# Kernel optimization log

Hardware: AMD Instinct MI355X
Metric: run time of the kernel (lower is better)

The kernel has to match this reference:

```python
import jax, jax.numpy as jnp
import numpy as np
import math

SCALE = 64.0
MARGIN = 0.5
EPS = 1e-07
COS_M = math.cos(MARGIN)
SIN_M = math.sin(MARGIN)
THRESHOLD = math.cos(math.pi - MARGIN)
MM = math.sin(math.pi - MARGIN) * MARGIN

N, D, C = 512, 512, 100000


def setup_inputs() -> dict:
    key = jax.random.key(0)
    k1, k2, k3 = jax.random.split(key, 3)
    x = jax.random.normal(k1, (N, D), dtype=jnp.float32)
    weight = jax.random.normal(k2, (C, D), dtype=jnp.float32)
    t = jnp.zeros((1,), dtype=jnp.float32)
    target = jax.random.randint(k3, (N,), 0, C, dtype=jnp.int64)
    return {"x": x, "weight": weight, "t": t, "target": target}


def reference(x, weight, t, target):
    # normalized linear -> cosine similarities [N, C]
    xn = x / jnp.linalg.norm(x, axis=1, keepdims=True)
    wn = weight / jnp.linalg.norm(weight, axis=1, keepdims=True)
    cos_theta = jnp.clip(jnp.einsum('nd,cd->nc', xn, wn), -1.0 + EPS, 1.0 - EPS)

    rows = jnp.arange(cos_theta.shape[0])
    target_logit = cos_theta[rows, target][:, None]            # [N, 1]
    sin_theta = jnp.sqrt(1.0 - target_logit * target_logit)
    cos_theta_m = target_logit * COS_M - sin_theta * SIN_M      # cos(theta + m)

    mask = cos_theta > cos_theta_m                              # hard examples
    final_target_logit = jnp.where(target_logit > THRESHOLD,
                                   cos_theta_m,
                                   target_logit - MM)

    # EMA buffer update (no-grad in torch)
    t_new = jax.lax.stop_gradient(target_logit.mean() * 0.01 + 0.99 * t)  # [1]

    # hard-example re-weighting: cos * (t + cos) where mask
    cos_theta = jnp.where(mask, cos_theta * (t_new[0] + cos_theta), cos_theta)
    # scatter margin-adjusted target logit into target column
    cos_theta = cos_theta.at[rows, target].set(final_target_logit[:, 0])

    logits = cos_theta * SCALE
    # cross entropy (mean)
    logp = jax.nn.log_softmax(logits, axis=-1)
    loss = -jnp.mean(logp[rows, target])
    return loss
```

## Files before the change

kernel.cpp:

```cpp
#include <hip/hip_runtime.h>
#include <hip/hip_bf16.h>
#include <stdint.h>

#define N_ROWS 512
#define D_DIM  512
#define C_CLS  100000

#define SCALE_F    64.0f
#define EPS_F      1e-7f
#define COS_M_F    0.8775825618903728f
#define SIN_M_F    0.4794255386042030f
#define THRESH_F  -0.8775825618903728f
#define MM_F       0.2397127693021015f
#define FIXMAX_F   65.0f

#define NG 391

#define XN8_OFF    0
#define TL_OFF     (XN8_OFF + 512*512)
#define CTM_OFF    (TL_OFF + 2048)
#define FTL_OFF    (CTM_OFF + 2048)
#define TNEW_OFF   (FTL_OFF + 2048)
#define XNORM_OFF  (TNEW_OFF + 256)
#define PSUM_OFF   (XNORM_OFF + 2048)
#define LOSSI_OFF  (PSUM_OFF + 512*NG*4)
#define WNB8_OFF   (LOSSI_OFF + 2048)

typedef __attribute__((ext_vector_type(4))) float f32x4;

#define GLOAD_LDS16(gp, lp) \
    __builtin_amdgcn_global_load_lds((const __attribute__((address_space(1))) void*)(gp), \
                                     (__attribute__((address_space(3))) void*)(lp), 16, 0, 0)

#if defined(__has_builtin)
#if __has_builtin(__builtin_amdgcn_cvt_pk_fp8_f32)
#define HAVE_CVT_FP8 1
#endif
#endif

__device__ inline unsigned char f2e4m3(float f) {
    union { float f; unsigned u; } a; a.f = f;
    unsigned s = (a.u >> 24) & 0x80u;
    float af = fabsf(f);
    if (af < 0.015625f) {
        int q = (int)(af * 512.0f + 0.5f);
        return (unsigned char)(s | (unsigned)q);
    }
    unsigned x = a.u & 0x7FFFFFFFu;
    unsigned r = x + 0x000FFFFFu + ((x >> 20) & 1u);
    int ec = (int)(r >> 23) - 127 + 7;
    unsigned m = (r >> 20) & 7u;
    if (ec > 15 || (ec == 15 && m == 7u)) return (unsigned char)(s | 0x7Eu);
    return (unsigned char)(s | ((unsigned)ec << 3) | m);
}

__device__ inline uint2 pack8_fp8(float f0, float f1, float f2, float f3,
                                  float f4, float f5, float f6, float f7) {
#ifdef HAVE_CVT_FP8
    int w0 = __builtin_amdgcn_cvt_pk_fp8_f32(f0, f1, 0, false);
    w0     = __builtin_amdgcn_cvt_pk_fp8_f32(f2, f3, w0, true);
    int w1 = __builtin_amdgcn_cvt_pk_fp8_f32(f4, f5, 0, false);
    w1     = __builtin_amdgcn_cvt_pk_fp8_f32(f6, f7, w1, true);
    uint2 r; r.x = (unsigned)w0; r.y = (unsigned)w1;
    return r;
#else
    union { unsigned char b[8]; uint2 q; } u;
    u.b[0]=f2e4m3(f0); u.b[1]=f2e4m3(f1); u.b[2]=f2e4m3(f2); u.b[3]=f2e4m3(f3);
    u.b[4]=f2e4m3(f4); u.b[5]=f2e4m3(f5); u.b[6]=f2e4m3(f6); u.b[7]=f2e4m3(f7);
    return u.q;
#endif
}

__device__ inline float wave_sum64(float v) {
    #pragma unroll
    for (int m = 1; m < 64; m <<= 1) v += __shfl_xor(v, m);
    return v;
}

__global__ void k_xnorm_fp8(const float* __restrict__ x,
                            unsigned char* __restrict__ xn8,
                            float* __restrict__ xnorm) {
    int row = blockIdx.x;
    int lane = threadIdx.x;
    const float* xr = x + row * D_DIM + lane * 8;
    float4 v0 = *(const float4*)(xr);
    float4 v1 = *(const float4*)(xr + 4);
    float s = v0.x*v0.x + v0.y*v0.y + v0.z*v0.z + v0.w*v0.w
            + v1.x*v1.x + v1.y*v1.y + v1.z*v1.z + v1.w*v1.w;
    s = wave_sum64(s);
    float nrm = sqrtf(s);
    if (lane == 0) xnorm[row] = nrm;
    float inv = 1.0f / nrm;
    uint2 q = pack8_fp8(v0.x*inv, v0.y*inv, v0.z*inv, v0.w*inv,
                        v1.x*inv, v1.y*inv, v1.z*inv, v1.w*inv);
    *(uint2*)(xn8 + row * D_DIM + lane * 8) = q;
}

__global__ void k_wnorm_fp8(const float* __restrict__ w,
                            unsigned char* __restrict__ wnb8) {
    int row = blockIdx.x * 4 + (threadIdx.x >> 6);
    int lane = threadIdx.x & 63;
    if (row < C_CLS) {
        const float* wr = w + (size_t)row * D_DIM + lane * 8;
        f32x4 v0 = __builtin_nontemporal_load((const f32x4*)(wr));
        f32x4 v1 = __builtin_nontemporal_load((const f32x4*)(wr + 4));
        float s = v0.x*v0.x + v0.y*v0.y + v0.z*v0.z + v0.w*v0.w
                + v1.x*v1.x + v1.y*v1.y + v1.z*v1.z + v1.w*v1.w;
        s = wave_sum64(s);
        float inv = rsqrtf(s);
        uint2 q = pack8_fp8(v0.x*inv, v0.y*inv, v0.z*inv, v0.w*inv,
                            v1.x*inv, v1.y*inv, v1.z*inv, v1.w*inv);
        *(uint2*)(wnb8 + (size_t)row * D_DIM + lane * 8) = q;
    } else {
        uint2 z = {0u, 0u};
        *(uint2*)(wnb8 + (size_t)row * D_DIM + lane * 8) = z;
    }
}

__global__ void k_tlogit(const float* __restrict__ x, const float* __restrict__ w,
                         const float* __restrict__ xnorm,
                         const int* __restrict__ target,
                         float* __restrict__ tl, float* __restrict__ ctm,
                         float* __restrict__ ftl) {
    int row = blockIdx.x;
    int lane = threadIdx.x;
    int tgt = target[row];
    const float* xr = x + row * D_DIM + lane * 8;
    const float* wr = w + (size_t)tgt * D_DIM + lane * 8;
    float4 a0 = *(const float4*)(xr),     a1 = *(const float4*)(xr + 4);
    float4 b0 = *(const float4*)(wr),     b1 = *(const float4*)(wr + 4);
    float s = a0.x*b0.x + a0.y*b0.y + a0.z*b0.z + a0.w*b0.w
            + a1.x*b1.x + a1.y*b1.y + a1.z*b1.z + a1.w*b1.w;
    float q = b0.x*b0.x + b0.y*b0.y + b0.z*b0.z + b0.w*b0.w
            + b1.x*b1.x + b1.y*b1.y + b1.z*b1.z + b1.w*b1.w;
    s = wave_sum64(s);
    q = wave_sum64(q);
    if (lane == 0) {
        float c = s / (xnorm[row] * sqrtf(q));
        c = fminf(fmaxf(c, -1.0f + EPS_F), 1.0f - EPS_F);
        float sn = sqrtf(fmaxf(1.0f - c * c, 0.0f));
        float cm = c * COS_M_F - sn * SIN_M_F;
        tl[row]  = c;
        ctm[row] = cm;
        ftl[row] = (c > THRESH_F) ? cm : (c - MM_F);
    }
}

__global__ void k_tnew(const float* __restrict__ tl, const float* __restrict__ t,
                       float* __restrict__ tnew) {
    __shared__ float s[512];
    int tid = threadIdx.x;
    s[tid] = tl[tid];
    __syncthreads();
    for (int off = 256; off > 0; off >>= 1) {
        if (tid < off) s[tid] += s[tid + off];
        __syncthreads();
    }
    if (tid == 0) tnew[0] = (s[0] / 512.0f) * 0.01f + 0.99f * t[0];
}

__global__ __launch_bounds__(512) void k_gemm_fp8(
        const unsigned char* __restrict__ xn8,
        const unsigned char* __restrict__ wnb8,
        const int* __restrict__ target,
        const float* __restrict__ ctm,
        const float* __restrict__ ftl,
        const float* __restrict__ tnew,
        float* __restrict__ psum) {
    __shared__ unsigned char As[64 * 512];
    __shared__ int   tgt_s[64];
    __shared__ float ctm_s[64];
    __shared__ float ftl_s[64];
    __shared__ float redS[8][64];

    int bx = blockIdx.x;
    int logical = (bx & 7) * 391 + (bx >> 3);
    int ng = logical >> 3, mb = logical & 7;
    int rowbase = mb * 64;

    int tid = threadIdx.x;
    int lane = tid & 63, wid = tid >> 6;
    int fr = lane & 15, rgrp = lane >> 4;
    int cb = ng * 256 + wid * 32;

    if (tid < 64) {
        int rg = rowbase + tid;
        tgt_s[tid] = target[rg];
        ctm_s[tid] = ctm[rg];
        ftl_s[tid] = ftl[rg];
    }

    const unsigned char* bptr[2];
    bool cvalid[2];
    #pragma unroll
    for (int j = 0; j < 2; j++) {
        int cgl = cb + j * 16 + fr;
        cvalid[j] = (cgl < C_CLS);
        bptr[j] = wnb8 + (size_t)cgl * D_DIM + rgrp * 8;
    }

    uint2 bv[6][2];
    #pragma unroll
    for (int d = 0; d < 6; d++)
        #pragma unroll
        for (int j = 0; j < 2; j++)
            bv[d][j] = *(const uint2*)(bptr[j] + d * 32);

    #pragma unroll
    for (int c2 = 0; c2 < 4; ++c2) {
        int lo = wid * 4096 + c2 * 1024;
        int o  = lo + lane * 16;
        int row = o >> 9;
        int b   = (o & 511) ^ ((row & 7) << 4);
        GLOAD_LDS16(xn8 + (size_t)(rowbase + row) * 512 + b, (char*)As + lo);
    }
    __syncthreads();

    float tn = tnew[0];
    int key = (fr & 7) << 4;

    f32x4 acc[4][2];
    #pragma unroll
    for (int m = 0; m < 4; m++)
        #pragma unroll
        for (int j = 0; j < 2; j++)
            acc[m][j] = (f32x4){0.f, 0.f, 0.f, 0.f};

    union LL { uint2 u; long long ll; };

    uint2 af[2][4];
    #pragma unroll
    for (int m = 0; m < 4; m++)
        af[0][m] = *(const uint2*)(As + (m * 16 + fr) * 512 + ((rgrp * 8) ^ key));

    #pragma unroll
    for (int kk = 0; kk < 16; ++kk) {
        int cur = kk & 1;
        if (kk < 15) {
            #pragma unroll
            for (int m = 0; m < 4; m++)
                af[cur ^ 1][m] = *(const uint2*)(As + (m * 16 + fr) * 512
                                 + (((kk + 1) * 32 + rgrp * 8) ^ key));
        }
        if (kk < 10) {
            #pragma unroll
            for (int j = 0; j < 2; j++)
                bv[(kk + 6) % 6][j] = *(const uint2*)(bptr[j] + (kk + 6) * 32);
        }
        __builtin_amdgcn_s_setprio(1);
        #pragma unroll
        for (int m = 0; m < 4; m++)
            #pragma unroll
            for (int j = 0; j < 2; j++) {
                LL a, b;
                a.u = af[cur][m];
                b.u = bv[kk % 6][j];
                acc[m][j] = __builtin_amdgcn_mfma_f32_16x16x32_fp8_fp8(
                                a.ll, b.ll, acc[m][j], 0, 0, 0);
            }
        __builtin_amdgcn_s_setprio(0);
    }

    #pragma unroll
    for (int m = 0; m < 4; m++) {
        #pragma unroll
        for (int reg = 0; reg < 4; reg++) {
            int rl = m * 16 + rgrp * 4 + reg;
            int tr = tgt_s[rl];
            float cm = ctm_s[rl];
            float ft = ftl_s[rl];
            float sm = 0.0f;
            #pragma unroll
            for (int j = 0; j < 2; j++) {
                int col = cb + j * 16 + fr;
                float c = acc[m][j][reg];
                c = fminf(fmaxf(c, -1.0f + EPS_F), 1.0f - EPS_F);
                float v = (c > cm) ? c * (tn + c) : c;
                v *= SCALE_F;
                v = (col == tr) ? ft * SCALE_F : v;
                v = cvalid[j] ? v : -3.0e38f;
                sm += __expf(v - FIXMAX_F);
            }
            #pragma unroll
            for (int msk = 1; msk < 16; msk <<= 1) sm += __shfl_xor(sm, msk);
            if (fr == 0) redS[wid][rl] = sm;
        }
    }
    __syncthreads();
    if (tid < 64) {
        float S = 0.0f;
        #pragma unroll
        for (int wv = 0; wv < 8; wv++) S += redS[wv][tid];
        psum[(size_t)(rowbase + tid) * NG + ng] = S;
    }
}

__global__ void k_rowlse_fix(const float* __restrict__ psum,
                             const float* __restrict__ ftl,
                             float* __restrict__ lossi) {
    int row = blockIdx.x, tid = threadIdx.x;
    float S = 0.0f;
    for (int nb = tid; nb < NG; nb += 256) S += psum[(size_t)row * NG + nb];
    __shared__ float sS[256];
    sS[tid] = S;
    __syncthreads();
    for (int off = 128; off > 0; off >>= 1) {
        if (tid < off) sS[tid] += sS[tid + off];
        __syncthreads();
    }
    if (tid == 0) lossi[row] = logf(sS[0]) + FIXMAX_F - SCALE_F * ftl[row];
}

__global__ void k_final(const float* __restrict__ lossi, float* __restrict__ out) {
    __shared__ float s[512];
    int tid = threadIdx.x;
    s[tid] = lossi[tid];
    __syncthreads();
    for (int off = 256; off > 0; off >>= 1) {
        if (tid < off) s[tid] += s[tid + off];
        __syncthreads();
    }
    if (tid == 0) out[0] = s[0] / 512.0f;
}

extern "C" void kernel_launch(void* const* d_in, const int* in_sizes, int n_in,
                              void* d_out, int out_size, void* d_ws, size_t ws_size,
                              hipStream_t stream) {
    const float* x      = (const float*)d_in[0];
    const float* w      = (const float*)d_in[1];
    const float* t      = (const float*)d_in[2];
    const int*   target = (const int*)d_in[3];

    char* ws = (char*)d_ws;
    unsigned char* xn8  = (unsigned char*)(ws + XN8_OFF);
    float* tl    = (float*)(ws + TL_OFF);
    float* ctm   = (float*)(ws + CTM_OFF);
    float* ftl   = (float*)(ws + FTL_OFF);
    float* tnew  = (float*)(ws + TNEW_OFF);
    float* xnorm = (float*)(ws + XNORM_OFF);
    float* psum  = (float*)(ws + PSUM_OFF);
    float* lossi = (float*)(ws + LOSSI_OFF);
    unsigned char* wnb8 = (unsigned char*)(ws + WNB8_OFF);
    float* out   = (float*)d_out;

    k_xnorm_fp8<<<dim3(N_ROWS), dim3(64), 0, stream>>>(x, xn8, xnorm);
    k_tlogit<<<dim3(N_ROWS), dim3(64), 0, stream>>>(x, w, xnorm, target, tl, ctm, ftl);
    k_tnew<<<dim3(1), dim3(512), 0, stream>>>(tl, t, tnew);
    k_wnorm_fp8<<<dim3((C_CLS + 3) / 4 + 6, 1), dim3(256), 0, stream>>>(w, wnb8);
    k_gemm_fp8<<<dim3(8 * NG), dim3(512), 0, stream>>>(xn8, wnb8, target, ctm, ftl, tnew, psum);
    k_rowlse_fix<<<dim3(N_ROWS), dim3(256), 0, stream>>>(psum, ftl, lossi);
    k_final<<<dim3(1), dim3(512), 0, stream>>>(lossi, out);
}
```

Before: 149.1 us.

## Fuse weight normalization and FP8 quantization into the GEMM kernel

Removes the separate weight-normalization kernel and its FP8 workspace copy. The GEMM now reads fp32 weights directly, quantizes raw weights to FP8 into double-buffered LDS, and accumulates each class's sum of squares on the fly. The inverse norm is applied to the accumulator in the epilogue. Each block now covers all 512 rows for 64 classes, so the large weight matrix is read once and the fp8 intermediate write and read are gone. The trade-off is that the full xn8 tile is re-staged from L2 by every block, there is a block-wide sync per K step, and the partial-sum buffer grows.

New measurement: 121.9 us. 1.22x faster.

```diff
diff --git a/kernel.cpp b/kernel.cpp
--- a/kernel.cpp
+++ b/kernel.cpp
@@ -14,7 +14,8 @@
 #define MM_F       0.2397127693021015f
 #define FIXMAX_F   65.0f
 
-#define NG 391
+#define NC  64
+#define NG2 1564
 
 #define XN8_OFF    0
 #define TL_OFF     (XN8_OFF + 512*512)
@@ -23,8 +24,7 @@
 #define TNEW_OFF   (FTL_OFF + 2048)
 #define XNORM_OFF  (TNEW_OFF + 256)
 #define PSUM_OFF   (XNORM_OFF + 2048)
-#define LOSSI_OFF  (PSUM_OFF + 512*NG*4)
-#define WNB8_OFF   (LOSSI_OFF + 2048)
+#define LOSSI_OFF  (PSUM_OFF + 512*NG2*4)
 
 typedef __attribute__((ext_vector_type(4))) float f32x4;
 
@@ -54,21 +54,24 @@
     return (unsigned char)(s | ((unsigned)ec << 3) | m);
 }
 
+__device__ inline unsigned pack4_fp8(float f0, float f1, float f2, float f3) {
+#ifdef HAVE_CVT_FP8
+    int q = __builtin_amdgcn_cvt_pk_fp8_f32(f0, f1, 0, false);
+    q     = __builtin_amdgcn_cvt_pk_fp8_f32(f2, f3, q, true);
+    return (unsigned)q;
+#else
+    union { unsigned char b[4]; unsigned u; } u;
+    u.b[0]=f2e4m3(f0); u.b[1]=f2e4m3(f1); u.b[2]=f2e4m3(f2); u.b[3]=f2e4m3(f3);
+    return u.u;
+#endif
+}
+
 __device__ inline uint2 pack8_fp8(float f0, float f1, float f2, float f3,
                                   float f4, float f5, float f6, float f7) {
-#ifdef HAVE_CVT_FP8
-    int w0 = __builtin_amdgcn_cvt_pk_fp8_f32(f0, f1, 0, false);
-    w0     = __builtin_amdgcn_cvt_pk_fp8_f32(f2, f3, w0, true);
-    int w1 = __builtin_amdgcn_cvt_pk_fp8_f32(f4, f5, 0, false);
-    w1     = __builtin_amdgcn_cvt_pk_fp8_f32(f6, f7, w1, true);
-    uint2 r; r.x = (unsigned)w0; r.y = (unsigned)w1;
+    uint2 r;
+    r.x = pack4_fp8(f0, f1, f2, f3);
+    r.y = pack4_fp8(f4, f5, f6, f7);
     return r;
-#else
-    union { unsigned char b[8]; uint2 q; } u;
-    u.b[0]=f2e4m3(f0); u.b[1]=f2e4m3(f1); u.b[2]=f2e4m3(f2); u.b[3]=f2e4m3(f3);
-    u.b[4]=f2e4m3(f4); u.b[5]=f2e4m3(f5); u.b[6]=f2e4m3(f6); u.b[7]=f2e4m3(f7);
-    return u.q;
-#endif
 }
 
 __device__ inline float wave_sum64(float v) {
@@ -94,27 +97,6 @@
     uint2 q = pack8_fp8(v0.x*inv, v0.y*inv, v0.z*inv, v0.w*inv,
                         v1.x*inv, v1.y*inv, v1.z*inv, v1.w*inv);
     *(uint2*)(xn8 + row * D_DIM + lane * 8) = q;
-}
-
-__global__ void k_wnorm_fp8(const float* __restrict__ w,
-                            unsigned char* __restrict__ wnb8) {
-    int row = blockIdx.x * 4 + (threadIdx.x >> 6);
-    int lane = threadIdx.x & 63;
-    if (row < C_CLS) {
-        const float* wr = w + (size_t)row * D_DIM + lane * 8;
-        f32x4 v0 = __builtin_nontemporal_load((const f32x4*)(wr));
-        f32x4 v1 = __builtin_nontemporal_load((const f32x4*)(wr + 4));
-        float s = v0.x*v0.x + v0.y*v0.y + v0.z*v0.z + v0.w*v0.w
-                + v1.x*v1.x + v1.y*v1.y + v1.z*v1.z + v1.w*v1.w;
-        s = wave_sum64(s);
-        float inv = rsqrtf(s);
-        uint2 q = pack8_fp8(v0.x*inv, v0.y*inv, v0.z*inv, v0.w*inv,
-                            v1.x*inv, v1.y*inv, v1.z*inv, v1.w*inv);
-        *(uint2*)(wnb8 + (size_t)row * D_DIM + lane * 8) = q;
-    } else {
-        uint2 z = {0u, 0u};
-        *(uint2*)(wnb8 + (size_t)row * D_DIM + lane * 8) = z;
-    }
 }
 
 __global__ void k_tlogit(const float* __restrict__ x, const float* __restrict__ w,
@@ -159,121 +141,132 @@
     if (tid == 0) tnew[0] = (s[0] / 512.0f) * 0.01f + 0.99f * t[0];
 }
 
-__global__ __launch_bounds__(512) void k_gemm_fp8(
+__global__ __launch_bounds__(512, 4) void k_fused(
         const unsigned char* __restrict__ xn8,
-        const unsigned char* __restrict__ wnb8,
+        const float* __restrict__ w,
         const int* __restrict__ target,
         const float* __restrict__ ctm,
         const float* __restrict__ ftl,
         const float* __restrict__ tnew,
         float* __restrict__ psum) {
-    __shared__ unsigned char As[64 * 512];
-    __shared__ int   tgt_s[64];
-    __shared__ float ctm_s[64];
-    __shared__ float ftl_s[64];
-    __shared__ float redS[8][64];
+    __shared__ unsigned char As[2][512 * 32];
+    __shared__ unsigned char Bs[2][64 * 32];
+    __shared__ float invS[64];
+    __shared__ int   tgt_s[512];
+    __shared__ float ctm_s[512];
+    __shared__ float ftl_s[512];
 
     int bx = blockIdx.x;
-    int logical = (bx & 7) * 391 + (bx >> 3);
-    int ng = logical >> 3, mb = logical & 7;
-    int rowbase = mb * 64;
-
+    int cb = bx * NC;
     int tid = threadIdx.x;
     int lane = tid & 63, wid = tid >> 6;
     int fr = lane & 15, rgrp = lane >> 4;
-    int cb = ng * 256 + wid * 32;
-
-    if (tid < 64) {
-        int rg = rowbase + tid;
-        tgt_s[tid] = target[rg];
-        ctm_s[tid] = ctm[rg];
-        ftl_s[tid] = ftl[rg];
-    }
-
-    const unsigned char* bptr[2];
-    bool cvalid[2];
-    #pragma unroll
-    for (int j = 0; j < 2; j++) {
-        int cgl = cb + j * 16 + fr;
-        cvalid[j] = (cgl < C_CLS);
-        bptr[j] = wnb8 + (size_t)cgl * D_DIM + rgrp * 8;
-    }
-
-    uint2 bv[6][2];
-    #pragma unroll
-    for (int d = 0; d < 6; d++)
-        #pragma unroll
-        for (int j = 0; j < 2; j++)
-            bv[d][j] = *(const uint2*)(bptr[j] + d * 32);
-
-    #pragma unroll
-    for (int c2 = 0; c2 < 4; ++c2) {
-        int lo = wid * 4096 + c2 * 1024;
-        int o  = lo + lane * 16;
-        int row = o >> 9;
-        int b   = (o & 511) ^ ((row & 7) << 4);
-        GLOAD_LDS16(xn8 + (size_t)(rowbase + row) * 512 + b, (char*)As + lo);
-    }
+    int wrow = wid * 64;
+
+    tgt_s[tid] = target[tid];
+    ctm_s[tid] = ctm[tid];
+    ftl_s[tid] = ftl[tid];
+
+    int brow  = tid >> 3;
+    int bslot = tid & 7;
+    int bclass = cb + brow;
+    bool brvalid = (bclass < C_CLS);
+    const float* bsrc = w + (size_t)(brvalid ? bclass : 0) * D_DIM + bslot * 4;
+
+    float sumsq = 0.0f;
+
+    #define STAGE_A(kk, buf)                                                  \
+        do {                                                                  \
+            _Pragma("unroll")                                                 \
+            for (int c = 0; c < 2; ++c) {                                     \
+                int lo = c * 8192 + wid * 1024;             \
+                int o  = lo + lane * 16;                                      \
+                int row = o >> 5, b = o & 31;                                 \
+                GLOAD_LDS16(xn8 + (size_t)row * 512 + (kk) * 32 + b,          \
+                            (char*)As[buf] + lo);                             \
+            }                                                                 \
+        } while (0)
+
+    #define STAGE_B(kk, buf)                                                  \
+        do {                                                                  \
+            float4 v_ = *(const float4*)(bsrc + (kk) * 32);                   \
+            sumsq += v_.x*v_.x + v_.y*v_.y + v_.z*v_.z + v_.w*v_.w;           \
+            *(unsigned*)(&Bs[buf][brow * 32 + bslot * 4]) =                   \
+                pack4_fp8(v_.x, v_.y, v_.z, v_.w);                            \
+        } while (0)
+
+    STAGE_A(0, 0);
+    STAGE_B(0, 0);
     __syncthreads();
 
     float tn = tnew[0];
-    int key = (fr & 7) << 4;
-
-    f32x4 acc[4][2];
+
+    f32x4 acc[4][4];
     #pragma unroll
     for (int m = 0; m < 4; m++)
         #pragma unroll
-        for (int j = 0; j < 2; j++)
+        for (int j = 0; j < 4; j++)
             acc[m][j] = (f32x4){0.f, 0.f, 0.f, 0.f};
 
     union LL { uint2 u; long long ll; };
 
-    uint2 af[2][4];
-    #pragma unroll
-    for (int m = 0; m < 4; m++)
-        af[0][m] = *(const uint2*)(As + (m * 16 + fr) * 512 + ((rgrp * 8) ^ key));
-
-    #pragma unroll
     for (int kk = 0; kk < 16; ++kk) {
         int cur = kk & 1;
         if (kk < 15) {
-            #pragma unroll
-            for (int m = 0; m < 4; m++)
-                af[cur ^ 1][m] = *(const uint2*)(As + (m * 16 + fr) * 512
-                                 + (((kk + 1) * 32 + rgrp * 8) ^ key));
+            STAGE_A(kk + 1, cur ^ 1);
+            STAGE_B(kk + 1, cur ^ 1);
         }
-        if (kk < 10) {
-            #pragma unroll
-            for (int j = 0; j < 2; j++)
-                bv[(kk + 6) % 6][j] = *(const uint2*)(bptr[j] + (kk + 6) * 32);
-        }
+        uint2 af[4], bf[4];
+        #pragma unroll
+        for (int m = 0; m < 4; m++)
+            af[m] = *(const uint2*)(&As[cur][(wrow + m * 16 + fr) * 32 + rgrp * 8]);
+        #pragma unroll
+        for (int j = 0; j < 4; j++)
+            bf[j] = *(const uint2*)(&Bs[cur][(j * 16 + fr) * 32 + rgrp * 8]);
         __builtin_amdgcn_s_setprio(1);
         #pragma unroll
         for (int m = 0; m < 4; m++)
             #pragma unroll
-            for (int j = 0; j < 2; j++) {
+            for (int j = 0; j < 4; j++) {
                 LL a, b;
-                a.u = af[cur][m];
-                b.u = bv[kk % 6][j];
+                a.u = af[m];
+                b.u = bf[j];
                 acc[m][j] = __builtin_amdgcn_mfma_f32_16x16x32_fp8_fp8(
                                 a.ll, b.ll, acc[m][j], 0, 0, 0);
             }
         __builtin_amdgcn_s_setprio(0);
-    }
-
+        __syncthreads();
+    }
+    #undef STAGE_A
+    #undef STAGE_B
+
+    float s2 = sumsq;
+    s2 += __shfl_xor(s2, 1);
+    s2 += __shfl_xor(s2, 2);
+    s2 += __shfl_xor(s2, 4);
+    if (bslot == 0) invS[brow] = rsqrtf(s2);
+    __syncthreads();
+
+    float inv[4];
+    bool cvalid[4];
+    #pragma unroll
+    for (int j = 0; j < 4; j++) {
+        inv[j] = invS[j * 16 + fr];
+        cvalid[j] = (cb + j * 16 + fr) < C_CLS;
+    }
     #pragma unroll
     for (int m = 0; m < 4; m++) {
         #pragma unroll
         for (int reg = 0; reg < 4; reg++) {
-            int rl = m * 16 + rgrp * 4 + reg;
+            int rl = wrow + m * 16 + rgrp * 4 + reg;
             int tr = tgt_s[rl];
             float cm = ctm_s[rl];
             float ft = ftl_s[rl];
             float sm = 0.0f;
             #pragma unroll
-            for (int j = 0; j < 2; j++) {
+            for (int j = 0; j < 4; j++) {
                 int col = cb + j * 16 + fr;
-                float c = acc[m][j][reg];
+                float c = acc[m][j][reg] * inv[j];
                 c = fminf(fmaxf(c, -1.0f + EPS_F), 1.0f - EPS_F);
                 float v = (c > cm) ? c * (tn + c) : c;
                 v *= SCALE_F;
@@ -283,15 +276,8 @@
             }
             #pragma unroll
             for (int msk = 1; msk < 16; msk <<= 1) sm += __shfl_xor(sm, msk);
-            if (fr == 0) redS[wid][rl] = sm;
+            if (fr == 0) psum[(size_t)rl * NG2 + bx] = sm;
         }
-    }
-    __syncthreads();
-    if (tid < 64) {
-        float S = 0.0f;
-        #pragma unroll
-        for (int wv = 0; wv < 8; wv++) S += redS[wv][tid];
-        psum[(size_t)(rowbase + tid) * NG + ng] = S;
     }
 }
 
@@ -300,7 +286,7 @@
                              float* __restrict__ lossi) {
     int row = blockIdx.x, tid = threadIdx.x;
     float S = 0.0f;
-    for (int nb = tid; nb < NG; nb += 256) S += psum[(size_t)row * NG + nb];
+    for (int nb = tid; nb < NG2; nb += 256) S += psum[(size_t)row * NG2 + nb];
     __shared__ float sS[256];
     sS[tid] = S;
     __syncthreads();
@@ -340,14 +326,12 @@
     float* xnorm = (float*)(ws + XNORM_OFF);
     float* psum  = (float*)(ws + PSUM_OFF);
     float* lossi = (float*)(ws + LOSSI_OFF);
-    unsigned char* wnb8 = (unsigned char*)(ws + WNB8_OFF);
     float* out   = (float*)d_out;
 
     k_xnorm_fp8<<<dim3(N_ROWS), dim3(64), 0, stream>>>(x, xn8, xnorm);
     k_tlogit<<<dim3(N_ROWS), dim3(64), 0, stream>>>(x, w, xnorm, target, tl, ctm, ftl);
     k_tnew<<<dim3(1), dim3(512), 0, stream>>>(tl, t, tnew);
-    k_wnorm_fp8<<<dim3((C_CLS + 3) / 4 + 6, 1), dim3(256), 0, stream>>>(w, wnb8);
-    k_gemm_fp8<<<dim3(8 * NG), dim3(512), 0, stream>>>(xn8, wnb8, target, ctm, ftl, tnew, psum);
+    k_fused<<<dim3(NG2), dim3(512), 0, stream>>>(xn8, w, target, ctm, ftl, tnew, psum);
     k_rowlse_fix<<<dim3(N_ROWS), dim3(256), 0, stream>>>(psum, ftl, lossi);
     k_final<<<dim3(1), dim3(512), 0, stream>>>(lossi, out);
 }
```
